# Kernel optimization log

Hardware: AMD Instinct MI355X
Metric: run time of the kernel (lower is better)

## Reference

```python
import jax, jax.numpy as jnp
import numpy as np

N = 50000
E = 800000
IN_C, HID, OUT_C, HEADS = 128, 32, 64, 4
NEG_SLOPE = 0.2


def setup_inputs() -> dict:
    key = jax.random.key(0)
    ks = jax.random.split(key, 10)
    x = jax.random.normal(ks[0], (N, IN_C), dtype=jnp.float32)
    edge_index = jax.random.randint(ks[1], (2, E), 0, N, dtype=jnp.int64)
    s = 0.05
    W1 = jax.random.normal(ks[2], (IN_C, HID), dtype=jnp.float32) * s
    b1 = jnp.zeros((HID,), dtype=jnp.float32)
    Wg = jax.random.normal(ks[3], (HID, HEADS * HID), dtype=jnp.float32) * s
    ag_src = jax.random.normal(ks[4], (HEADS, HID), dtype=jnp.float32) * s
    ag_dst = jax.random.normal(ks[5], (HEADS, HID), dtype=jnp.float32) * s
    bg = jnp.zeros((HID,), dtype=jnp.float32)
    W2 = jax.random.normal(ks[6], (HID, OUT_C), dtype=jnp.float32) * s
    b2 = jnp.zeros((OUT_C,), dtype=jnp.float32)
    return {"x": x, "edge_index": edge_index, "W1": W1, "b1": b1,
            "Wg": Wg, "ag_src": ag_src, "ag_dst": ag_dst, "bg": bg,
            "W2": W2, "b2": b2}


def _add_self_loops(edge_index, n):
    loop = jnp.arange(n, dtype=edge_index.dtype)
    return jnp.concatenate([edge_index, jnp.stack([loop, loop])], axis=1)


def _gcn(x, src, dst, W, b, n):
    # PyG GCNConv: symmetric normalization with self-loops, scatter-add
    xw = x @ W  # [N, F]
    deg = jnp.zeros((n,), xw.dtype).at[dst].add(1.0)  # in-degree incl self-loops
    dinv = jax.lax.rsqrt(deg)
    norm = dinv[src] * dinv[dst]  # [E']
    msg = xw[src] * norm[:, None]  # [E', F]
    out = jax.ops.segment_sum(msg, dst, num_segments=n)
    return out + b


def _gat(x, src, dst, Wg, a_src, a_dst, b, n):
    # PyG GATConv, concat=False (mean over heads), leaky_relu slope 0.2
    h = (x @ Wg).reshape(n, HEADS, HID)  # [N, H, D]
    al_s = jnp.einsum('nhd,hd->nh', h, a_src)  # [N, H]
    al_d = jnp.einsum('nhd,hd->nh', h, a_dst)
    logits = jax.nn.leaky_relu(al_s[src] + al_d[dst], NEG_SLOPE)  # [E', H]
    # segment softmax over incoming edges of each dst node
    m = jax.ops.segment_max(logits, dst, num_segments=n)
    e = jnp.exp(logits - m[dst])
    denom = jax.ops.segment_sum(e, dst, num_segments=n)
    alpha = e / denom[dst]  # [E', H]
    msg = h[src] * alpha[:, :, None]  # [E', H, D]
    out = jax.ops.segment_sum(msg, dst, num_segments=n)  # [N, H, D]
    return out.mean(axis=1) + b


def reference(x, edge_index, W1, b1, Wg, ag_src, ag_dst, bg, W2, b2):
    ei = _add_self_loops(edge_index, N)
    src, dst = ei[0], ei[1]
    h = jax.nn.relu(_gcn(x, src, dst, W1, b1, N))
    h = jax.nn.relu(_gat(h, src, dst, Wg, ag_src, ag_dst, bg, N))
    return _gcn(h, src, dst, W2, b2, N)
```

## Files before the change

kernel.cpp:

```cpp
#include <hip/hip_runtime.h>
#include <hip/hip_bf16.h>

#define N_NODES 50000
#define N_EDGES 800000
#define EP (N_EDGES + N_NODES)
#define IN_C 128
#define HID 32
#define OUT_C 64
#define HEADS 4
#define NEG_SLOPE 0.2f

#define NPB 128
#define K_BUCKETS ((N_NODES + NPB - 1) / NPB)

typedef unsigned int uint32;
typedef __attribute__((ext_vector_type(8))) short bf16x8;
typedef __attribute__((ext_vector_type(4))) float f32x4;

__device__ __forceinline__ float bf_lo(uint32 u) { return __uint_as_float(u << 16); }
__device__ __forceinline__ float bf_hi(uint32 u) { return __uint_as_float(u & 0xffff0000u); }
__device__ __forceinline__ uint32 f2bf(float f) {
    uint32 u = __float_as_uint(f);
    return (u + 0x7fffu + ((u >> 16) & 1u)) >> 16;
}
__device__ __forceinline__ uint32 pack_bf2(float a, float b) {
    return f2bf(a) | (f2bf(b) << 16);
}

__global__ __launch_bounds__(512) void k_init2(int* __restrict__ gcnt,
                                               const float* __restrict__ Wg,
                                               const float* __restrict__ ags,
                                               const float* __restrict__ agd,
                                               float* __restrict__ wals,
                                               float* __restrict__ wald,
                                               const float* __restrict__ W2,
                                               uint32* __restrict__ wgB,
                                               uint32* __restrict__ w2B) {
    int t = threadIdx.x;
    if (t < K_BUCKETS + 1) gcnt[t] = 0;
    if (t < 256) {
        int c = t & 127;
        int h = c >> 5, k = c & 31;
        const float* a = (t < 128) ? ags : agd;
        float acc = 0.f;
#pragma unroll
        for (int d = 0; d < 32; d++) acc += Wg[k * 128 + h * 32 + d] * a[h * 32 + d];
        if (t < 128) wals[c] = acc; else wald[c] = acc;
    }
    for (int i = t; i < 2048; i += 512) {
        int tile = i >> 8;
        int T = tile >> 2, kt = tile & 3;
        int r = i & 255;
        int L = r >> 2, di = r & 3;
        int k0 = kt * 32 + (L >> 4) * 8 + 2 * di;
        int k1 = k0 + 1;
        int n = T * 16 + (L & 15);
        float a = Wg[(k0 & 31) * 128 + (k0 >> 5) * 32 + n];
        float b = Wg[(k1 & 31) * 128 + (k1 >> 5) * 32 + n];
        wgB[i] = pack_bf2(a, b);
    }
    for (int i = t; i < 1024; i += 512) {
        int T = i >> 8;
        int r = i & 255;
        int L = r >> 2, di = r & 3;
        int k0 = (L >> 4) * 8 + 2 * di;
        int n = T * 16 + (L & 15);
        w2B[i] = pack_bf2(W2[k0 * 64 + n], W2[(k0 + 1) * 64 + n]);
    }
}


__global__ __launch_bounds__(256) void k_bcount(const int* __restrict__ ei,
                                                int* __restrict__ gcnt) {
    __shared__ int h[K_BUCKETS];
    int t = threadIdx.x;
    for (int i = t; i < K_BUCKETS; i += 256) h[i] = 0;
    __syncthreads();
    int base = blockIdx.x * 4096;
    int dd[16];
#pragma unroll
    for (int k = 0; k < 16; k++) {
        int e = base + k * 256 + t;
        dd[k] = (e < N_EDGES) ? ei[N_EDGES + e] : -1;
    }
#pragma unroll
    for (int k = 0; k < 16; k++)
        if (dd[k] >= 0) atomicAdd(&h[dd[k] >> 7], 1);
    __syncthreads();
    for (int i = t; i < K_BUCKETS; i += 256)
        if (h[i]) atomicAdd(&gcnt[i], h[i]);
}

__global__ __launch_bounds__(512) void k_bscan(const int* __restrict__ gcnt,
                                               int* __restrict__ gbase,
                                               int* __restrict__ gcursor) {
    __shared__ int sd[512];
    int t = threadIdx.x;
    int v = (t < K_BUCKETS) ? gcnt[t] : 0;
    sd[t] = v;
    __syncthreads();
    for (int off = 1; off < 512; off <<= 1) {
        int x = (t >= off) ? sd[t - off] : 0;
        __syncthreads();
        sd[t] += x;
        __syncthreads();
    }
    if (t < K_BUCKETS) {
        int excl = sd[t] - v;
        gbase[t] = excl;
        gcursor[t] = excl;
    }
    if (t == 0) gbase[K_BUCKETS] = sd[K_BUCKETS - 1];
}

__global__ __launch_bounds__(256) void k_bucket(const int* __restrict__ ei,
                                                int* __restrict__ gcursor,
                                                uint32* __restrict__ gpairs) {
    __shared__ int cnt[K_BUCKETS];
    __shared__ int bas[K_BUCKETS];
    int t = threadIdx.x;
    for (int i = t; i < K_BUCKETS; i += 256) cnt[i] = 0;
    __syncthreads();
    int base = blockIdx.x * 2048;
    int ss[8], dd[8], ml[8];
#pragma unroll
    for (int k = 0; k < 8; k++) {
        int e = base + k * 256 + t;
        ss[k] = (e < N_EDGES) ? ei[e] : -1;
        dd[k] = (e < N_EDGES) ? ei[N_EDGES + e] : 0;
    }
#pragma unroll
    for (int k = 0; k < 8; k++)
        if (ss[k] >= 0) ml[k] = atomicAdd(&cnt[dd[k] >> 7], 1);
    __syncthreads();
    for (int i = t; i < K_BUCKETS; i += 256)
        bas[i] = cnt[i] ? atomicAdd(&gcursor[i], cnt[i]) : 0;
    __syncthreads();
#pragma unroll
    for (int k = 0; k < 8; k++)
        if (ss[k] >= 0)
            gpairs[bas[dd[k] >> 7] + ml[k]] = ((uint32)ss[k] << 7) | (uint32)(dd[k] & 127);
}

__global__ __launch_bounds__(256) void k_node(const uint32* __restrict__ gpairs,
                                              const int* __restrict__ gbase,
                                              int* __restrict__ offs,
                                              float* __restrict__ dinv,
                                              int* __restrict__ srcs) {
    __shared__ int cnt[NPB];
    __shared__ int scn[NPB];
    __shared__ int cur[NPB];
    int t = threadIdx.x;
    int b = blockIdx.x;
    int lo = b << 7;
    int nn = N_NODES - lo; if (nn > NPB) nn = NPB;
    int pb = gbase[b], pe = gbase[b + 1];
    if (t < NPB) cnt[t] = 0;
    __syncthreads();
    for (int i = pb + t; i < pe; i += 256)
        atomicAdd(&cnt[gpairs[i] & 127], 1);
    __syncthreads();
    if (t < NPB) scn[t] = cnt[t];
    __syncthreads();
    for (int off = 1; off < NPB; off <<= 1) {
        int x = 0;
        if (t >= off && t < NPB) x = scn[t - off];
        __syncthreads();
        if (t < NPB) scn[t] += x;
        __syncthreads();
    }
    if (t < nn) {
        int excl = scn[t] - cnt[t];
        int o = pb + excl + lo + t;
        offs[lo + t] = o;
        cur[t] = o;
        dinv[lo + t] = rsqrtf((float)(cnt[t] + 1));
        srcs[pb + scn[t] + lo + t] = lo + t;
    }
    if (b == K_BUCKETS - 1 && t == 0) offs[N_NODES] = pe + N_NODES;
    __syncthreads();
    for (int i = pb + t; i < pe; i += 256) {
        uint32 u = gpairs[i];
        int pos = atomicAdd(&cur[u & 127], 1);
        srcs[pos] = (int)(u >> 7);
    }
}

__global__ __launch_bounds__(256) void k_gemm1(const float* __restrict__ x,
                                               const float* __restrict__ W1,
                                               const float* __restrict__ dinv,
                                               uint32* __restrict__ xw1) {
    __shared__ float wl[IN_C * HID];
    __shared__ float xl[8 * IN_C];
    int t = threadIdx.x;
    for (int i = t; i < IN_C * HID; i += 256) {
        int k = i >> 5, f = i & 31;
        wl[(k >> 1) * 64 + f * 2 + (k & 1)] = W1[i];
    }
    int nb = blockIdx.x * 8;
    const float4* x4 = (const float4*)(x + (size_t)nb * IN_C);
    ((float4*)xl)[t] = x4[t];
    __syncthreads();
    int g = t >> 5, f = t & 31;
    const float2* xr = (const float2*)(xl + g * IN_C);
    const float2* wp = (const float2*)wl;
    float acc = 0.f;
#pragma unroll 16
    for (int k2 = 0; k2 < 64; k2++) {
        float2 xv = xr[k2];
        float2 wv = wp[k2 * 32 + f];
        acc += xv.x * wv.x + xv.y * wv.y;
    }
    float v = acc * dinv[nb + g];
    float vn = __shfl_xor(v, 1, 64);
    if ((f & 1) == 0) xw1[(size_t)(nb + g) * 16 + (f >> 1)] = pack_bf2(v, vn);
}

__global__ __launch_bounds__(256) void k_gather1(const uint32* __restrict__ xw1,
                                                 const int* __restrict__ offs,
                                                 const int* __restrict__ srcs,
                                                 const float* __restrict__ dinv,
                                                 const float* __restrict__ b1,
                                                 const float* __restrict__ wals,
                                                 const float* __restrict__ wald,
                                                 char* __restrict__ rec) {
    int t = threadIdx.x;
    int l16 = t & 15;
    int n = blockIdx.x * 16 + (t >> 4);
    int s0 = offs[n], s1 = offs[n + 1];
    const char* xb = (const char*)xw1 + l16 * 4;
    float a0 = 0.f, a1 = 0.f, a2 = 0.f, a3 = 0.f;
    int j = s0;
    for (; j + 1 < s1; j += 2) {
        uint32 uA = *(const uint32*)(xb + ((uint32)srcs[j] << 6));
        uint32 uB = *(const uint32*)(xb + ((uint32)srcs[j + 1] << 6));
        a0 += bf_lo(uA); a1 += bf_hi(uA);
        a2 += bf_lo(uB); a3 += bf_hi(uB);
    }
    if (j < s1) {
        uint32 uA = *(const uint32*)(xb + ((uint32)srcs[j] << 6));
        a0 += bf_lo(uA); a1 += bf_hi(uA);
    }
    float dn = dinv[n];
    float2 b = ((const float2*)b1)[l16];
    float vx = (a0 + a2) * dn + b.x;
    float vy = (a1 + a3) * dn + b.y;
    vx = vx > 0.f ? vx : 0.f;
    vy = vy > 0.f ? vy : 0.f;
    char* rn = rec + (size_t)n * 128;
    *(uint32*)(rn + 64 + l16 * 4) = pack_bf2(vx, vy);

    float ps0, ps1, ps2, ps3, pd0, pd1, pd2, pd3;
    {
        float2 w0 = ((const float2*)wals)[0 * 16 + l16];
        float2 w1 = ((const float2*)wals)[1 * 16 + l16];
        float2 w2 = ((const float2*)wals)[2 * 16 + l16];
        float2 w3 = ((const float2*)wals)[3 * 16 + l16];
        ps0 = vx * w0.x + vy * w0.y;
        ps1 = vx * w1.x + vy * w1.y;
        ps2 = vx * w2.x + vy * w2.y;
        ps3 = vx * w3.x + vy * w3.y;
        float2 u0 = ((const float2*)wald)[0 * 16 + l16];
        float2 u1 = ((const float2*)wald)[1 * 16 + l16];
        float2 u2 = ((const float2*)wald)[2 * 16 + l16];
        float2 u3 = ((const float2*)wald)[3 * 16 + l16];
        pd0 = vx * u0.x + vy * u0.y;
        pd1 = vx * u1.x + vy * u1.y;
        pd2 = vx * u2.x + vy * u2.y;
        pd3 = vx * u3.x + vy * u3.y;
    }
#pragma unroll
    for (int m = 1; m < 16; m <<= 1) {
        ps0 += __shfl_xor(ps0, m, 16); ps1 += __shfl_xor(ps1, m, 16);
        ps2 += __shfl_xor(ps2, m, 16); ps3 += __shfl_xor(ps3, m, 16);
        pd0 += __shfl_xor(pd0, m, 16); pd1 += __shfl_xor(pd1, m, 16);
        pd2 += __shfl_xor(pd2, m, 16); pd3 += __shfl_xor(pd3, m, 16);
    }
    if (l16 == 0) {
        float4* r4 = (float4*)rn;
        r4[0] = make_float4(__expf(ps0), __expf(ps1), __expf(ps2), __expf(ps3));
        r4[1] = make_float4(__expf(NEG_SLOPE * ps0), __expf(NEG_SLOPE * ps1),
                            __expf(NEG_SLOPE * ps2), __expf(NEG_SLOPE * ps3));
        r4[2] = make_float4(__expf(pd0), __expf(pd1), __expf(pd2), __expf(pd3));
        r4[3] = make_float4(__expf(NEG_SLOPE * pd0), __expf(NEG_SLOPE * pd1),
                            __expf(NEG_SLOPE * pd2), __expf(NEG_SLOPE * pd3));
    }
}

__global__ __launch_bounds__(512) void k_gat_agg(const char* __restrict__ rec,
                                                 const int* __restrict__ offs,
                                                 const int* __restrict__ srcs,
                                                 const uint32* __restrict__ wgB,
                                                 const float* __restrict__ bg,
                                                 const float* __restrict__ dinv,
                                                 uint32* __restrict__ h2s) {
    __shared__ __align__(16) uint32 gl[16][64];
    int t = threadIdx.x;
    int l32 = t & 31;
    int g8 = t >> 5;
    int n = blockIdx.x * 16 + g8;
    int l16 = l32 & 15;
    int par = l32 >> 4;
    int s0 = offs[n], s1 = offs[n + 1];
    const float4* dn4 = (const float4*)(rec + (size_t)n * 128);
    float4 d1 = dn4[2];
    float4 d2 = dn4[3];
    uint32 hoff = 64 + l16 * 4;

    float g00 = 0.f, g01 = 0.f, g10 = 0.f, g11 = 0.f;
    float g20 = 0.f, g21 = 0.f, g30 = 0.f, g31 = 0.f;
    float ss0 = 0.f, ss1 = 0.f, ss2 = 0.f, ss3 = 0.f;

#define GAT_EDGE(J)                                                            \
    {                                                                          \
        uint32 off = (uint32)srcs[J] << 7;                                     \
        float4 e1 = *(const float4*)(rec + off);                               \
        float4 e2 = *(const float4*)(rec + off + 16);                          \
        uint32 u = *(const uint32*)(rec + off + hoff);                         \
        float flo = bf_lo(u), fhi = bf_hi(u);                                  \
        float p, q, w;                                                         \
        p = e1.x * d1.x; q = e2.x * d2.x; w = p > 1.f ? p : q;                 \
        ss0 += w; g00 += w * flo; g01 += w * fhi;                              \
        p = e1.y * d1.y; q = e2.y * d2.y; w = p > 1.f ? p : q;                 \
        ss1 += w; g10 += w * flo; g11 += w * fhi;                              \
        p = e1.z * d1.z; q = e2.z * d2.z; w = p > 1.f ? p : q;                 \
        ss2 += w; g20 += w * flo; g21 += w * fhi;                              \
        p = e1.w * d1.w; q = e2.w * d2.w; w = p > 1.f ? p : q;                 \
        ss3 += w; g30 += w * flo; g31 += w * fhi;                              \
    }

    int j = s0 + par;
    for (; j + 2 < s1; j += 4) {
        GAT_EDGE(j);
        GAT_EDGE(j + 2);
    }
    if (j < s1) GAT_EDGE(j);
#undef GAT_EDGE

    ss0 += __shfl_xor(ss0, 16, 64); ss1 += __shfl_xor(ss1, 16, 64);
    ss2 += __shfl_xor(ss2, 16, 64); ss3 += __shfl_xor(ss3, 16, 64);
    g00 += __shfl_xor(g00, 16, 64); g01 += __shfl_xor(g01, 16, 64);
    g10 += __shfl_xor(g10, 16, 64); g11 += __shfl_xor(g11, 16, 64);
    g20 += __shfl_xor(g20, 16, 64); g21 += __shfl_xor(g21, 16, 64);
    g30 += __shfl_xor(g30, 16, 64); g31 += __shfl_xor(g31, 16, 64);
    float i0 = 0.25f / ss0, i1 = 0.25f / ss1, i2 = 0.25f / ss2, i3 = 0.25f / ss3;
    if (l32 < 16) {
        gl[g8][0 * 16 + l16] = pack_bf2(g00 * i0, g01 * i0);
        gl[g8][1 * 16 + l16] = pack_bf2(g10 * i1, g11 * i1);
        gl[g8][2 * 16 + l16] = pack_bf2(g20 * i2, g21 * i2);
        gl[g8][3 * 16 + l16] = pack_bf2(g30 * i3, g31 * i3);
    }
    __syncthreads();
    if (t < 64) {
        int L = t;
        int mA = L & 15;
        int quad = L >> 4;
        int nbase = blockIdx.x * 16;
        float dn0 = dinv[nbase + quad * 4 + 0];
        float dn1 = dinv[nbase + quad * 4 + 1];
        float dn2 = dinv[nbase + quad * 4 + 2];
        float dn3 = dinv[nbase + quad * 4 + 3];
#pragma unroll
        for (int T = 0; T < 2; T++) {
            f32x4 acc = {0.f, 0.f, 0.f, 0.f};
#pragma unroll
            for (int kt = 0; kt < 4; kt++) {
                bf16x8 af = *(const bf16x8*)&gl[mA][kt * 16 + quad * 4];
                bf16x8 bf = *(const bf16x8*)(wgB + (size_t)((T * 4 + kt) * 64 + L) * 4);
                acc = __builtin_amdgcn_mfma_f32_16x16x32_bf16(af, bf, acc, 0, 0, 0);
            }
            int d = T * 16 + (L & 15);
            float bgd = bg[d];
            float dns[4] = {dn0, dn1, dn2, dn3};
#pragma unroll
            for (int r = 0; r < 4; r++) {
                int node = nbase + quad * 4 + r;
                float v = acc[r] + bgd;
                v = v > 0.f ? v : 0.f;
                v *= dns[r];
                float vn = __shfl_xor(v, 1, 64);
                if ((d & 1) == 0)
                    h2s[(size_t)node * 16 + (d >> 1)] = pack_bf2(v, vn);
            }
        }
    }
}

__global__ __launch_bounds__(256) void k_gather2(const uint32* __restrict__ h2s,
                                                 const int* __restrict__ offs,
                                                 const int* __restrict__ srcs,
                                                 const uint32* __restrict__ w2B,
                                                 const float* __restrict__ dinv,
                                                 const float* __restrict__ b2,
                                                 float* __restrict__ out) {
    __shared__ __align__(16) uint32 gbf[16][16];
    int t = threadIdx.x;
    int l16 = t & 15;
    int g16 = t >> 4;
    int n = blockIdx.x * 16 + g16;
    int s0 = offs[n], s1 = offs[n + 1];
    const char* xb = (const char*)h2s + l16 * 4;
    float a0 = 0.f, a1 = 0.f, a2 = 0.f, a3 = 0.f;
    int j = s0;
    for (; j + 1 < s1; j += 2) {
        uint32 uA = *(const uint32*)(xb + ((uint32)srcs[j] << 6));
        uint32 uB = *(const uint32*)(xb + ((uint32)srcs[j + 1] << 6));
        a0 += bf_lo(uA); a1 += bf_hi(uA);
        a2 += bf_lo(uB); a3 += bf_hi(uB);
    }
    if (j < s1) {
        uint32 uA = *(const uint32*)(xb + ((uint32)srcs[j] << 6));
        a0 += bf_lo(uA); a1 += bf_hi(uA);
    }
    gbf[g16][l16] = pack_bf2(a0 + a2, a1 + a3);
    __syncthreads();
    if (t < 64) {
        int L = t;
        int quad = L >> 4;
        int nbase = blockIdx.x * 16;
        float dns[4];
#pragma unroll
        for (int r = 0; r < 4; r++) dns[r] = dinv[nbase + quad * 4 + r];
        bf16x8 af = *(const bf16x8*)&gbf[L & 15][quad * 4];
#pragma unroll
        for (int T = 0; T < 4; T++) {
            bf16x8 bf = *(const bf16x8*)(w2B + (size_t)(T * 64 + L) * 4);
            f32x4 acc = {0.f, 0.f, 0.f, 0.f};
            acc = __builtin_amdgcn_mfma_f32_16x16x32_bf16(af, bf, acc, 0, 0, 0);
            int d = T * 16 + (L & 15);
            float b2d = b2[d];
#pragma unroll
            for (int r = 0; r < 4; r++) {
                int node = nbase + quad * 4 + r;
                out[(size_t)node * OUT_C + d] = acc[r] * dns[r] + b2d;
            }
        }
    }
}

extern "C" void kernel_launch(void* const* d_in, const int* in_sizes, int n_in,
                              void* d_out, int out_size, void* d_ws, size_t ws_size,
                              hipStream_t stream) {
    const float* x   = (const float*)d_in[0];
    const int*   ei  = (const int*)d_in[1];
    const float* W1  = (const float*)d_in[2];
    const float* b1  = (const float*)d_in[3];
    const float* Wg  = (const float*)d_in[4];
    const float* ags = (const float*)d_in[5];
    const float* agd = (const float*)d_in[6];
    const float* bg  = (const float*)d_in[7];
    const float* W2  = (const float*)d_in[8];
    const float* b2  = (const float*)d_in[9];
    float* out = (float*)d_out;

    char* p = (char*)d_ws;
    auto alloc = [&](size_t bytes) -> void* {
        void* r = (void*)p;
        p += (bytes + 255) & ~(size_t)255;
        return r;
    };
    float*  dinv    = (float*)alloc((size_t)N_NODES * 4);
    int*    offs    = (int*)  alloc((size_t)(N_NODES + 1) * 4);
    int*    gcnt    = (int*)  alloc((size_t)(K_BUCKETS + 1) * 4);
    int*    gbase   = (int*)  alloc((size_t)(K_BUCKETS + 1) * 4);
    int*    gcursor = (int*)  alloc((size_t)(K_BUCKETS + 1) * 4);
    int*    srcs    = (int*)  alloc((size_t)EP * 4);
    uint32* gpairs  = (uint32*)alloc((size_t)N_EDGES * 4);
    uint32* xw1     = (uint32*)alloc((size_t)N_NODES * 16 * 4);
    char*   rec     = (char*) alloc((size_t)N_NODES * 128);
    float*  wals    = (float*)alloc(128 * 4);
    float*  wald    = (float*)alloc(128 * 4);
    uint32* wgB     = (uint32*)alloc(2048 * 4);
    uint32* w2B     = (uint32*)alloc(1024 * 4);
    uint32* h2s     = (uint32*)alloc((size_t)N_NODES * 16 * 4);

    k_init2<<<1, 512, 0, stream>>>(gcnt, Wg, ags, agd, wals, wald, W2, wgB, w2B);
    k_bcount<<<(N_EDGES + 4095) / 4096, 256, 0, stream>>>(ei, gcnt);
    k_bscan<<<1, 512, 0, stream>>>(gcnt, gbase, gcursor);
    k_bucket<<<(N_EDGES + 2047) / 2048, 256, 0, stream>>>(ei, gcursor, gpairs);
    k_node<<<K_BUCKETS, 256, 0, stream>>>(gpairs, gbase, offs, dinv, srcs);

    k_gemm1<<<N_NODES / 8, 256, 0, stream>>>(x, W1, dinv, xw1);
    k_gather1<<<N_NODES / 16, 256, 0, stream>>>(xw1, offs, srcs, dinv, b1,
                                                wals, wald, rec);

    k_gat_agg<<<N_NODES / 16, 512, 0, stream>>>(rec, offs, srcs, wgB, bg, dinv, h2s);

    k_gather2<<<N_NODES / 16, 256, 0, stream>>>(h2s, offs, srcs, w2B, dinv, b2, out);
}
```

Baseline: 218.8 us.

## Degree-sort nodes per bucket, unroll gathers by four, compute GAT exp per edge

k_node now bitonic-sorts the 128 nodes of each bucket by in-degree and writes a permutation. The gather and aggregation kernels use it so that nodes with similar degree share a wavefront, which is meant to cut lane divergence in the edge loops. The GCN gather loops are unrolled by four with more independent accumulators for memory-level parallelism. The GAT record now stores raw attention logits instead of precomputed exponentials and computes exp(leaky_relu) per edge, which reads 16 bytes of logits per edge instead of 32 at the price of extra transcendental work. The permutation also scatters output writes and adds an indirection load.

```diff
diff --git a/kernel.cpp b/kernel.cpp
--- a/kernel.cpp
+++ b/kernel.cpp
@@ -146,10 +146,12 @@
                                               const int* __restrict__ gbase,
                                               int* __restrict__ offs,
                                               float* __restrict__ dinv,
-                                              int* __restrict__ srcs) {
+                                              int* __restrict__ srcs,
+                                              int* __restrict__ perm) {
     __shared__ int cnt[NPB];
     __shared__ int scn[NPB];
     __shared__ int cur[NPB];
+    __shared__ unsigned skey[NPB];
     int t = threadIdx.x;
     int b = blockIdx.x;
     int lo = b << 7;
@@ -184,6 +186,25 @@
         int pos = atomicAdd(&cur[u & 127], 1);
         srcs[pos] = (int)(u >> 7);
     }
+    if (t < NPB)
+        skey[t] = (t < nn) ? (((unsigned)cnt[t] << 7) | (unsigned)t)
+                           : (0x7fffff80u | (unsigned)t);
+    __syncthreads();
+    for (int k = 2; k <= NPB; k <<= 1) {
+        for (int jj = k >> 1; jj > 0; jj >>= 1) {
+            if (t < NPB) {
+                int ixj = t ^ jj;
+                if (ixj > t) {
+                    unsigned a = skey[t], bb = skey[ixj];
+                    if (((t & k) == 0) ? (a > bb) : (a < bb)) {
+                        skey[t] = bb; skey[ixj] = a;
+                    }
+                }
+            }
+            __syncthreads();
+        }
+    }
+    if (t < nn) perm[lo + t] = lo + (int)(skey[t] & 127u);
 }
 
 __global__ __launch_bounds__(256) void k_gemm1(const float* __restrict__ x,
@@ -219,6 +240,7 @@
 __global__ __launch_bounds__(256) void k_gather1(const uint32* __restrict__ xw1,
                                                  const int* __restrict__ offs,
                                                  const int* __restrict__ srcs,
+                                                 const int* __restrict__ perm,
                                                  const float* __restrict__ dinv,
                                                  const float* __restrict__ b1,
                                                  const float* __restrict__ wals,
@@ -226,29 +248,34 @@
                                                  char* __restrict__ rec) {
     int t = threadIdx.x;
     int l16 = t & 15;
-    int n = blockIdx.x * 16 + (t >> 4);
+    int n = perm[blockIdx.x * 16 + (t >> 4)];
     int s0 = offs[n], s1 = offs[n + 1];
     const char* xb = (const char*)xw1 + l16 * 4;
     float a0 = 0.f, a1 = 0.f, a2 = 0.f, a3 = 0.f;
+    float a4 = 0.f, a5 = 0.f, a6 = 0.f, a7 = 0.f;
     int j = s0;
-    for (; j + 1 < s1; j += 2) {
+    for (; j + 3 < s1; j += 4) {
         uint32 uA = *(const uint32*)(xb + ((uint32)srcs[j] << 6));
         uint32 uB = *(const uint32*)(xb + ((uint32)srcs[j + 1] << 6));
+        uint32 uC = *(const uint32*)(xb + ((uint32)srcs[j + 2] << 6));
+        uint32 uD = *(const uint32*)(xb + ((uint32)srcs[j + 3] << 6));
         a0 += bf_lo(uA); a1 += bf_hi(uA);
         a2 += bf_lo(uB); a3 += bf_hi(uB);
-    }
-    if (j < s1) {
+        a4 += bf_lo(uC); a5 += bf_hi(uC);
+        a6 += bf_lo(uD); a7 += bf_hi(uD);
+    }
+    for (; j < s1; ++j) {
         uint32 uA = *(const uint32*)(xb + ((uint32)srcs[j] << 6));
         a0 += bf_lo(uA); a1 += bf_hi(uA);
     }
     float dn = dinv[n];
     float2 b = ((const float2*)b1)[l16];
-    float vx = (a0 + a2) * dn + b.x;
-    float vy = (a1 + a3) * dn + b.y;
+    float vx = ((a0 + a2) + (a4 + a6)) * dn + b.x;
+    float vy = ((a1 + a3) + (a5 + a7)) * dn + b.y;
     vx = vx > 0.f ? vx : 0.f;
     vy = vy > 0.f ? vy : 0.f;
     char* rn = rec + (size_t)n * 128;
-    *(uint32*)(rn + 64 + l16 * 4) = pack_bf2(vx, vy);
+    *(uint32*)(rn + l16 * 4) = pack_bf2(vx, vy);
 
     float ps0, ps1, ps2, ps3, pd0, pd1, pd2, pd3;
     {
@@ -278,18 +305,15 @@
     }
     if (l16 == 0) {
         float4* r4 = (float4*)rn;
-        r4[0] = make_float4(__expf(ps0), __expf(ps1), __expf(ps2), __expf(ps3));
-        r4[1] = make_float4(__expf(NEG_SLOPE * ps0), __expf(NEG_SLOPE * ps1),
-                            __expf(NEG_SLOPE * ps2), __expf(NEG_SLOPE * ps3));
-        r4[2] = make_float4(__expf(pd0), __expf(pd1), __expf(pd2), __expf(pd3));
-        r4[3] = make_float4(__expf(NEG_SLOPE * pd0), __expf(NEG_SLOPE * pd1),
-                            __expf(NEG_SLOPE * pd2), __expf(NEG_SLOPE * pd3));
+        r4[4] = make_float4(ps0, ps1, ps2, ps3);
+        r4[5] = make_float4(pd0, pd1, pd2, pd3);
     }
 }
 
 __global__ __launch_bounds__(512) void k_gat_agg(const char* __restrict__ rec,
                                                  const int* __restrict__ offs,
                                                  const int* __restrict__ srcs,
+                                                 const int* __restrict__ perm,
                                                  const uint32* __restrict__ wgB,
                                                  const float* __restrict__ bg,
                                                  const float* __restrict__ dinv,
@@ -298,14 +322,12 @@
     int t = threadIdx.x;
     int l32 = t & 31;
     int g8 = t >> 5;
-    int n = blockIdx.x * 16 + g8;
+    int n = perm[blockIdx.x * 16 + g8];
     int l16 = l32 & 15;
     int par = l32 >> 4;
     int s0 = offs[n], s1 = offs[n + 1];
-    const float4* dn4 = (const float4*)(rec + (size_t)n * 128);
-    float4 d1 = dn4[2];
-    float4 d2 = dn4[3];
-    uint32 hoff = 64 + l16 * 4;
+    float4 dv = ((const float4*)(rec + (size_t)n * 128))[5];
+    uint32 hoff = l16 * 4;
 
     float g00 = 0.f, g01 = 0.f, g10 = 0.f, g11 = 0.f;
     float g20 = 0.f, g21 = 0.f, g30 = 0.f, g31 = 0.f;
@@ -314,18 +336,17 @@
 #define GAT_EDGE(J)                                                            \
     {                                                                          \
         uint32 off = (uint32)srcs[J] << 7;                                     \
-        float4 e1 = *(const float4*)(rec + off);                               \
-        float4 e2 = *(const float4*)(rec + off + 16);                          \
+        float4 ev = *(const float4*)(rec + off + 64);                          \
         uint32 u = *(const uint32*)(rec + off + hoff);                         \
         float flo = bf_lo(u), fhi = bf_hi(u);                                  \
-        float p, q, w;                                                         \
-        p = e1.x * d1.x; q = e2.x * d2.x; w = p > 1.f ? p : q;                 \
+        float tt, w;                                                           \
+        tt = ev.x + dv.x; w = __expf(fmaxf(tt, NEG_SLOPE * tt));               \
         ss0 += w; g00 += w * flo; g01 += w * fhi;                              \
-        p = e1.y * d1.y; q = e2.y * d2.y; w = p > 1.f ? p : q;                 \
+        tt = ev.y + dv.y; w = __expf(fmaxf(tt, NEG_SLOPE * tt));               \
         ss1 += w; g10 += w * flo; g11 += w * fhi;                              \
-        p = e1.z * d1.z; q = e2.z * d2.z; w = p > 1.f ? p : q;                 \
+        tt = ev.z + dv.z; w = __expf(fmaxf(tt, NEG_SLOPE * tt));               \
         ss2 += w; g20 += w * flo; g21 += w * fhi;                              \
-        p = e1.w * d1.w; q = e2.w * d2.w; w = p > 1.f ? p : q;                 \
+        tt = ev.w + dv.w; w = __expf(fmaxf(tt, NEG_SLOPE * tt));               \
         ss3 += w; g30 += w * flo; g31 += w * fhi;                              \
     }
 
@@ -356,10 +377,13 @@
         int mA = L & 15;
         int quad = L >> 4;
         int nbase = blockIdx.x * 16;
-        float dn0 = dinv[nbase + quad * 4 + 0];
-        float dn1 = dinv[nbase + quad * 4 + 1];
-        float dn2 = dinv[nbase + quad * 4 + 2];
-        float dn3 = dinv[nbase + quad * 4 + 3];
+        int pn[4];
+        float dns[4];
+#pragma unroll
+        for (int r = 0; r < 4; r++) {
+            pn[r] = perm[nbase + quad * 4 + r];
+            dns[r] = dinv[pn[r]];
+        }
 #pragma unroll
         for (int T = 0; T < 2; T++) {
             f32x4 acc = {0.f, 0.f, 0.f, 0.f};
@@ -371,16 +395,14 @@
             }
             int d = T * 16 + (L & 15);
             float bgd = bg[d];
-            float dns[4] = {dn0, dn1, dn2, dn3};
 #pragma unroll
             for (int r = 0; r < 4; r++) {
-                int node = nbase + quad * 4 + r;
                 float v = acc[r] + bgd;
                 v = v > 0.f ? v : 0.f;
                 v *= dns[r];
                 float vn = __shfl_xor(v, 1, 64);
                 if ((d & 1) == 0)
-                    h2s[(size_t)node * 16 + (d >> 1)] = pack_bf2(v, vn);
+                    h2s[(size_t)pn[r] * 16 + (d >> 1)] = pack_bf2(v, vn);
             }
         }
     }
@@ -389,6 +411,7 @@
 __global__ __launch_bounds__(256) void k_gather2(const uint32* __restrict__ h2s,
                                                  const int* __restrict__ offs,
                                                  const int* __restrict__ srcs,
+                                                 const int* __restrict__ perm,
                                                  const uint32* __restrict__ w2B,
                                                  const float* __restrict__ dinv,
                                                  const float* __restrict__ b2,
@@ -397,30 +420,39 @@
     int t = threadIdx.x;
     int l16 = t & 15;
     int g16 = t >> 4;
-    int n = blockIdx.x * 16 + g16;
+    int n = perm[blockIdx.x * 16 + g16];
     int s0 = offs[n], s1 = offs[n + 1];
     const char* xb = (const char*)h2s + l16 * 4;
     float a0 = 0.f, a1 = 0.f, a2 = 0.f, a3 = 0.f;
+    float a4 = 0.f, a5 = 0.f, a6 = 0.f, a7 = 0.f;
     int j = s0;
-    for (; j + 1 < s1; j += 2) {
+    for (; j + 3 < s1; j += 4) {
         uint32 uA = *(const uint32*)(xb + ((uint32)srcs[j] << 6));
         uint32 uB = *(const uint32*)(xb + ((uint32)srcs[j + 1] << 6));
+        uint32 uC = *(const uint32*)(xb + ((uint32)srcs[j + 2] << 6));
+        uint32 uD = *(const uint32*)(xb + ((uint32)srcs[j + 3] << 6));
         a0 += bf_lo(uA); a1 += bf_hi(uA);
         a2 += bf_lo(uB); a3 += bf_hi(uB);
-    }
-    if (j < s1) {
+        a4 += bf_lo(uC); a5 += bf_hi(uC);
+        a6 += bf_lo(uD); a7 += bf_hi(uD);
+    }
+    for (; j < s1; ++j) {
         uint32 uA = *(const uint32*)(xb + ((uint32)srcs[j] << 6));
         a0 += bf_lo(uA); a1 += bf_hi(uA);
     }
-    gbf[g16][l16] = pack_bf2(a0 + a2, a1 + a3);
+    gbf[g16][l16] = pack_bf2((a0 + a2) + (a4 + a6), (a1 + a3) + (a5 + a7));
     __syncthreads();
     if (t < 64) {
         int L = t;
         int quad = L >> 4;
         int nbase = blockIdx.x * 16;
+        int pn[4];
         float dns[4];
 #pragma unroll
-        for (int r = 0; r < 4; r++) dns[r] = dinv[nbase + quad * 4 + r];
+        for (int r = 0; r < 4; r++) {
+            pn[r] = perm[nbase + quad * 4 + r];
+            dns[r] = dinv[pn[r]];
+        }
         bf16x8 af = *(const bf16x8*)&gbf[L & 15][quad * 4];
 #pragma unroll
         for (int T = 0; T < 4; T++) {
@@ -431,8 +463,7 @@
             float b2d = b2[d];
 #pragma unroll
             for (int r = 0; r < 4; r++) {
-                int node = nbase + quad * 4 + r;
-                out[(size_t)node * OUT_C + d] = acc[r] * dns[r] + b2d;
+                out[(size_t)pn[r] * OUT_C + d] = acc[r] * dns[r] + b2d;
             }
         }
     }
@@ -473,18 +504,21 @@
     uint32* wgB     = (uint32*)alloc(2048 * 4);
     uint32* w2B     = (uint32*)alloc(1024 * 4);
     uint32* h2s     = (uint32*)alloc((size_t)N_NODES * 16 * 4);
+    int*    perm    = (int*)  alloc((size_t)N_NODES * 4);
 
     k_init2<<<1, 512, 0, stream>>>(gcnt, Wg, ags, agd, wals, wald, W2, wgB, w2B);
     k_bcount<<<(N_EDGES + 4095) / 4096, 256, 0, stream>>>(ei, gcnt);
     k_bscan<<<1, 512, 0, stream>>>(gcnt, gbase, gcursor);
     k_bucket<<<(N_EDGES + 2047) / 2048, 256, 0, stream>>>(ei, gcursor, gpairs);
-    k_node<<<K_BUCKETS, 256, 0, stream>>>(gpairs, gbase, offs, dinv, srcs);
+    k_node<<<K_BUCKETS, 256, 0, stream>>>(gpairs, gbase, offs, dinv, srcs, perm);
 
     k_gemm1<<<N_NODES / 8, 256, 0, stream>>>(x, W1, dinv, xw1);
-    k_gather1<<<N_NODES / 16, 256, 0, stream>>>(xw1, offs, srcs, dinv, b1,
+    k_gather1<<<N_NODES / 16, 256, 0, stream>>>(xw1, offs, srcs, perm, dinv, b1,
                                                 wals, wald, rec);
 
-    k_gat_agg<<<N_NODES / 16, 512, 0, stream>>>(rec, offs, srcs, wgB, bg, dinv, h2s);
-
-    k_gather2<<<N_NODES / 16, 256, 0, stream>>>(h2s, offs, srcs, w2B, dinv, b2, out);
-}
+    k_gat_agg<<<N_NODES / 16, 512, 0, stream>>>(rec, offs, srcs, perm, wgB, bg,
+                                                dinv, h2s);
+
+    k_gather2<<<N_NODES / 16, 256, 0, stream>>>(h2s, offs, srcs, perm, w2B,
+                                                dinv, b2, out);
+}
```

New measurement: 219.8 us. About the same (+0.5%).
